# Optimization experiments

Measured on AMD Instinct MI355X. Metric: run time of the kernel, lower is better.

Reference implementation:

```python
import jax, jax.numpy as jnp
import numpy as np

N_HEAD = 16

def setup_inputs() -> dict:
    key = jax.random.key(0)
    k1, k2, k3 = jax.random.split(key, 3)
    B, T, C = 2, 2048, 2048
    x = jax.random.normal(k1, (B, T, C), dtype=jnp.float32)
    # torch Linear weights are [out, in]; init with small scale for stability
    w_attn = jax.random.normal(k2, (3 * C, C), dtype=jnp.float32) * 0.02
    b_attn = jnp.zeros((3 * C,), dtype=jnp.float32)
    w_proj = jax.random.normal(k3, (C, C), dtype=jnp.float32) * 0.02
    b_proj = jnp.zeros((C,), dtype=jnp.float32)
    return {"x": x, "w_attn": w_attn, "b_attn": b_attn, "w_proj": w_proj, "b_proj": b_proj}

def reference(x, w_attn, b_attn, w_proj, b_proj):
    B, T, C = x.shape
    nh = N_HEAD
    hs = C // nh
    # fused QKV projection (torch Linear: x @ W^T + b)
    qkv = x @ w_attn.T + b_attn                      # [B, T, 3C]
    q, k, v = jnp.split(qkv, 3, axis=2)
    # [B, nh, T, hs]
    q = q.reshape(B, T, nh, hs).transpose(0, 2, 1, 3)
    k = k.reshape(B, T, nh, hs).transpose(0, 2, 1, 3)
    v = v.reshape(B, T, nh, hs).transpose(0, 2, 1, 3)
    # causal scaled dot-product attention
    scale = 1.0 / jnp.sqrt(jnp.asarray(hs, dtype=x.dtype))
    logits = jnp.einsum("bhqd,bhkd->bhqk", q, k) * scale  # [B, nh, T, T]
    causal = jnp.tril(jnp.ones((T, T), dtype=bool))
    logits = jnp.where(causal, logits, jnp.finfo(logits.dtype).min)
    attn = jax.nn.softmax(logits, axis=-1)
    y = jnp.einsum("bhqk,bhkd->bhqd", attn, v)       # [B, nh, T, hs]
    y = y.transpose(0, 2, 1, 3).reshape(B, T, C)
    # output projection (resid_dropout is identity in eval / p=0)
    y = y @ w_proj.T + b_proj
    return y
```

## Files before the change

### kernel.cpp

```cpp
#include <hip/hip_runtime.h>
#include <stdint.h>

typedef __bf16 bf16_t;
typedef __bf16 bf16x8 __attribute__((ext_vector_type(8)));
typedef float f32x4 __attribute__((ext_vector_type(4)));
typedef unsigned short us16x8 __attribute__((ext_vector_type(8)));

#define MFMA16(a, b, c) __builtin_amdgcn_mfma_f32_16x16x32_bf16(a, b, c, 0, 0, 0)
#define BAR() __builtin_amdgcn_s_barrier()
#define PRIO1() __builtin_amdgcn_s_setprio(1)
#define PRIO0() __builtin_amdgcn_s_setprio(0)
#define LGKM0()                                        \
  do {                                                 \
    asm volatile("s_waitcnt lgkmcnt(0)" ::: "memory"); \
    __builtin_amdgcn_sched_barrier(0);                 \
  } while (0)
#define VMCNT(n)                                          \
  do {                                                    \
    asm volatile("s_waitcnt vmcnt(" #n ")" ::: "memory"); \
    __builtin_amdgcn_sched_barrier(0);                    \
  } while (0)

__device__ __forceinline__ void stage16(const bf16_t* g, bf16_t* l) {
  __builtin_amdgcn_global_load_lds((__attribute__((address_space(1))) void*)g,
                                   (__attribute__((address_space(3))) void*)l, 16, 0, 0);
}

__global__ __launch_bounds__(256) void cvt_all(const float* __restrict__ x,
                                               const float* __restrict__ wa,
                                               const float* __restrict__ wp,
                                               bf16_t* __restrict__ xb,
                                               bf16_t* __restrict__ wab,
                                               bf16_t* __restrict__ wpb) {
  int i = blockIdx.x * 256 + threadIdx.x;
  const float* src;
  bf16_t* dst;
  if (i < 1048576) {
    src = x + (size_t)i * 8;
    dst = xb + (size_t)i * 8;
  } else if (i < 2621440) {
    size_t j = (size_t)(i - 1048576) * 8;
    src = wa + j;
    dst = wab + j;
  } else {
    size_t j = (size_t)(i - 2621440) * 8;
    src = wp + j;
    dst = wpb + j;
  }
  const f32x4* p = (const f32x4*)src;
  f32x4 a = p[0], b = p[1];
  bf16x8 o;
  o[0] = (bf16_t)a[0]; o[1] = (bf16_t)a[1]; o[2] = (bf16_t)a[2]; o[3] = (bf16_t)a[3];
  o[4] = (bf16_t)b[0]; o[5] = (bf16_t)b[1]; o[6] = (bf16_t)b[2]; o[7] = (bf16_t)b[3];
  *(bf16x8*)dst = o;
}

template <int OUT_BF16>
__global__ __launch_bounds__(256, 2) void gemm_w128p(const bf16_t* __restrict__ A,
                                                     const bf16_t* __restrict__ B,
                                                     const float* __restrict__ bias,
                                                     void* __restrict__ Cout,
                                                     int M, int N, int K) {
  __shared__ bf16_t SA[3 * 256 * 32];
  __shared__ bf16_t SB[3 * 128 * 32];
  const int tid = threadIdx.x;
  const int l = tid & 63, w = tid >> 6;
  const int l15 = l & 15, l4 = l >> 4;
  const int wm = w >> 1, wn = w & 1;
  const int nbn = N >> 7;
  const int nbm = M >> 8;
  const int total = nbm * nbn;
  const int bnpc = nbn >> 3;

  const int r0 = tid >> 2;
  const int scol = (((tid & 3) ^ ((r0 >> 1) & 3)) << 3);
  const size_t K64 = (size_t)64 * K;

  const int swz = (l4 ^ ((l15 >> 1) & 3)) << 3;
  int aoff[8], boff[4];
#pragma unroll
  for (int i = 0; i < 8; ++i) aoff[i] = (wm * 128 + i * 16 + l15) * 32 + swz;
#pragma unroll
  for (int i = 0; i < 4; ++i) boff[i] = (wn * 64 + i * 16 + l15) * 32 + swz;

  const int nk = K >> 5;

  for (int wk = blockIdx.x; wk < total; wk += gridDim.x) {
    const int c = wk & 7, rr0 = wk >> 3;
    const int bm = rr0 / bnpc;
    const int bn = c * bnpc + rr0 % bnpc;

    const bf16_t* gA = A + (size_t)(bm * 256 + r0) * K + scol;
    const bf16_t* gB = B + (size_t)(bn * 128 + r0) * K + scol;

    f32x4 acc[8][4] = {};

    auto STAGE = [&](int t2, int buf) {
      const size_t ko = (size_t)t2 * 32;
      stage16(gA + ko, SA + buf * 8192 + tid * 8);
      stage16(gA + K64 + ko, SA + buf * 8192 + 2048 + tid * 8);
      stage16(gA + 2 * K64 + ko, SA + buf * 8192 + 4096 + tid * 8);
      stage16(gA + 3 * K64 + ko, SA + buf * 8192 + 6144 + tid * 8);
      stage16(gB + ko, SB + buf * 4096 + tid * 8);
      stage16(gB + K64 + ko, SB + buf * 4096 + 2048 + tid * 8);
    };

    auto TILE = [&](int t, int bufR, int bufS) {
      const int t2 = (t + 2 < nk) ? t + 2 : nk - 1;
      STAGE(t2, bufS);
      bf16x8 aR[8], bR[4];
#pragma unroll
      for (int i = 0; i < 8; ++i) aR[i] = *(const bf16x8*)(SA + bufR * 8192 + aoff[i]);
#pragma unroll
      for (int i = 0; i < 4; ++i) bR[i] = *(const bf16x8*)(SB + bufR * 4096 + boff[i]);
      VMCNT(6);
      BAR();
      LGKM0();
      PRIO1();
#pragma unroll
      for (int mi = 0; mi < 8; ++mi)
#pragma unroll
        for (int ni = 0; ni < 4; ++ni)
          acc[mi][ni] = MFMA16(aR[mi], bR[ni], acc[mi][ni]);
      PRIO0();
      BAR();
    };

    STAGE(0, 0);
    STAGE(1, 1);
    VMCNT(6);
    BAR();

    for (int t = 0; t < nk - 1; t += 3) {
      TILE(t, 0, 2);
      TILE(t + 1, 1, 0);
      TILE(t + 2, 2, 1);
    }
    TILE(nk - 1, 0, 2);
    VMCNT(0);

    const int rbase = bm * 256 + wm * 128 + (l4 << 2);
    const int cbase = bn * 128 + wn * 64 + l15;
#pragma unroll
    for (int ni = 0; ni < 4; ++ni) {
      float bv = bias[cbase + ni * 16];
#pragma unroll
      for (int mi = 0; mi < 8; ++mi)
#pragma unroll
        for (int rr = 0; rr < 4; ++rr) {
          float v = acc[mi][ni][rr] + bv;
          size_t off = (size_t)(rbase + mi * 16 + rr) * N + (cbase + ni * 16);
          if (OUT_BF16) ((bf16_t*)Cout)[off] = (bf16_t)v;
          else ((float*)Cout)[off] = v;
        }
    }
  }
}

__global__ __launch_bounds__(256, 2) void attn_fwd(const bf16_t* __restrict__ qkv,
                                                   bf16_t* __restrict__ att) {
  __shared__ bf16_t Kt[2][64 * 128];
  __shared__ bf16_t Vt[2][128 * 64];
  __shared__ bf16_t Pw[4][16 * 64];

  int bid = blockIdx.x;
  int pair = bid >> 5, bh = bid & 31;
  int h = bh & 15, b = bh >> 4;
  int tid = threadIdx.x;
  int l = tid & 63, w = tid >> 6;
  int l15 = l & 15, l4 = l >> 4, l7 = l & 7;
  const size_t LD = 6144;
  const bf16_t* base = qkv + (size_t)b * 2048 * LD;

  us16x8 va[2], vb[2];

  auto loadV = [&](int kb) {
    const bf16_t* vg = base + (size_t)kb * LD + 4096 + h * 128;
#pragma unroll
    for (int p = 0; p < 2; ++p) {
      int g = p * 256 + tid;
      int kvp = (g >> 4) << 1;
      int d0 = (g & 15) << 3;
      va[p] = *(const us16x8*)(vg + (size_t)kvp * LD + d0);
      vb[p] = *(const us16x8*)(vg + (size_t)(kvp + 1) * LD + d0);
    }
  };
  auto stageK = [&](int kb, int buf) {
    const bf16_t* kg = base + (size_t)kb * LD + 2048 + h * 128;
#pragma unroll
    for (int i = 0; i < 4; ++i) {
      int e = i * 256 + tid;
      int row = e >> 4, blk = e & 15;
      int src = (blk ^ (row & 7)) << 3;
      stage16(kg + (size_t)row * LD + src, &Kt[buf][e * 8]);
    }
  };
  auto writeV = [&](int buf) {
#pragma unroll
    for (int p = 0; p < 2; ++p) {
      int g = p * 256 + tid;
      int kvp = (g >> 4) << 1;
      int d0 = (g & 15) << 3;
      int k8 = kvp >> 3, kr = kvp & 7;
#pragma unroll
      for (int j = 0; j < 8; ++j) {
        int d = d0 + j;
        int swzv = k8 ^ ((d ^ (d >> 3)) & 7);
        unsigned pack = (unsigned)va[p][j] | ((unsigned)vb[p][j] << 16);
        *(unsigned*)(&Vt[buf][d * 64 + swzv * 8 + kr]) = pack;
      }
    }
  };

#pragma unroll 1
  for (int phase = 0; phase < 2; ++phase) {
    int qt = phase ? 31 - pair : pair;
    int q0 = qt << 6;
    int wq0 = q0 + w * 16;

    bf16x8 qf[4];
#pragma unroll
    for (int kk = 0; kk < 4; ++kk)
      qf[kk] = *(const bf16x8*)(base + (size_t)(wq0 + l15) * LD + h * 128 + kk * 32 + l4 * 8);

    f32x4 acc[8] = {};
    float mrow[4], lrow[4];
#pragma unroll
    for (int r = 0; r < 4; ++r) { mrow[r] = -1e30f; lrow[r] = 0.f; }

    int nkt = qt + 1;

    loadV(0);
    stageK(0, 0);
    VMCNT(4);
    writeV(0);
    LGKM0();
    VMCNT(0);
    BAR();

#pragma unroll 1
    for (int kt = 0; kt < nkt; ++kt) {
      const int cur = kt & 1, nxt = cur ^ 1;
      const bool pf = (kt + 1 < nkt);
      const int kb = kt << 6;
      if (pf) {
        loadV((kt + 1) << 6);
        stageK((kt + 1) << 6, nxt);
      }

      f32x4 s[4] = {};
      PRIO1();
#pragma unroll
      for (int kk = 0; kk < 4; ++kk) {
        int blk = (kk * 4 + l4) ^ l7;
#pragma unroll
        for (int n = 0; n < 4; ++n) {
          bf16x8 kf = *(const bf16x8*)(&Kt[cur][(n * 16 + l15) * 128 + blk * 8]);
          s[n] = MFMA16(qf[kk], kf, s[n]);
        }
      }
      PRIO0();

      const float sc = 0.08838834764831845f;
      bool needMask = (kb + 63) > wq0;
      float scf[4];
#pragma unroll
      for (int r = 0; r < 4; ++r) {
        int q = wq0 + (l4 << 2) + r;
#pragma unroll
        for (int n = 0; n < 4; ++n) {
          float v = s[n][r] * sc;
          if (needMask && (kb + n * 16 + l15) > q) v = -1e30f;
          s[n][r] = v;
        }
        float mx = fmaxf(fmaxf(s[0][r], s[1][r]), fmaxf(s[2][r], s[3][r]));
        mx = fmaxf(mx, __shfl_xor(mx, 1));
        mx = fmaxf(mx, __shfl_xor(mx, 2));
        mx = fmaxf(mx, __shfl_xor(mx, 4));
        mx = fmaxf(mx, __shfl_xor(mx, 8));
        float mn = fmaxf(mrow[r], mx);
        float sf = __expf(mrow[r] - mn);
        mrow[r] = mn;
        scf[r] = sf;
        float rs = 0.f;
#pragma unroll
        for (int n = 0; n < 4; ++n) {
          float pv = __expf(s[n][r] - mn);
          s[n][r] = pv;
          rs += pv;
        }
        rs += __shfl_xor(rs, 1);
        rs += __shfl_xor(rs, 2);
        rs += __shfl_xor(rs, 4);
        rs += __shfl_xor(rs, 8);
        lrow[r] = lrow[r] * sf + rs;
      }

      if (pf) {
        VMCNT(4);
        writeV(nxt);
      }

#pragma unroll
      for (int nd = 0; nd < 8; ++nd)
#pragma unroll
        for (int r = 0; r < 4; ++r)
          acc[nd][r] *= scf[r];
#pragma unroll
      for (int n = 0; n < 4; ++n) {
        int cb8 = n * 2 + (l15 >> 3);
#pragma unroll
        for (int r = 0; r < 4; ++r) {
          int row = (l4 << 2) + r;
          Pw[w][row * 64 + ((cb8 ^ (row & 7)) << 3) + l7] = (bf16_t)s[n][r];
        }
      }

      PRIO1();
#pragma unroll
      for (int kk2 = 0; kk2 < 2; ++kk2) {
        bf16x8 pa = *(const bf16x8*)(&Pw[w][l15 * 64 + (((kk2 * 4 + l4) ^ l7) << 3)]);
#pragma unroll
        for (int nd = 0; nd < 8; ++nd) {
          int d = nd * 16 + l15;
          int swzv = (kk2 * 4 + l4) ^ ((d ^ (d >> 3)) & 7);
          bf16x8 bv = *(const bf16x8*)(&Vt[cur][d * 64 + swzv * 8]);
          acc[nd] = MFMA16(pa, bv, acc[nd]);
        }
      }
      PRIO0();

      LGKM0();
      VMCNT(0);
      BAR();
    }

#pragma unroll
    for (int r = 0; r < 4; ++r) {
      float inv = 1.0f / lrow[r];
      size_t ro = (size_t)(b * 2048 + wq0 + (l4 << 2) + r) * 2048 + h * 128;
#pragma unroll
      for (int nd = 0; nd < 8; ++nd)
        att[ro + nd * 16 + l15] = (bf16_t)(acc[nd][r] * inv);
    }
  }
}

extern "C" void kernel_launch(void* const* d_in, const int* in_sizes, int n_in,
                              void* d_out, int out_size, void* d_ws, size_t ws_size,
                              hipStream_t stream) {
  (void)in_sizes; (void)n_in; (void)out_size; (void)ws_size;
  const float* x = (const float*)d_in[0];
  const float* w_attn = (const float*)d_in[1];
  const float* b_attn = (const float*)d_in[2];
  const float* w_proj = (const float*)d_in[3];
  const float* b_proj = (const float*)d_in[4];
  float* out = (float*)d_out;

  char* ws = (char*)d_ws;
  bf16_t* xb  = (bf16_t*)(ws);
  bf16_t* wab = (bf16_t*)(ws + 16777216);
  bf16_t* wpb = (bf16_t*)(ws + 41943040);
  bf16_t* qkv = (bf16_t*)(ws + 50331648);
  bf16_t* att = xb;

  cvt_all<<<12288, 256, 0, stream>>>(x, w_attn, w_proj, xb, wab, wpb);

  gemm_w128p<1><<<512, 256, 0, stream>>>(xb, wab, b_attn, qkv, 4096, 6144, 2048);

  attn_fwd<<<512, 256, 0, stream>>>(qkv, att);

  gemm_w128p<0><<<256, 256, 0, stream>>>(att, wpb, b_proj, out, 4096, 2048, 2048);
}
```

Baseline: 296.9 us.

## Use 128-row query tiles per block and drop double-buffered K/V pipeline

The attention kernel now gives each block one 128-row query tile, with each wave holding 32 rows (two 16-row MFMA tiles), so every K/V fragment read from LDS is reused across two query tiles. The old two-phase pairing of 64-row tiles and the double-buffered asynchronous K/V prefetch are replaced by a single-buffered load, sync, compute loop, and the P scratch uses padded rows instead of an XOR swizzle. Blocks are balanced by pairing query tile p with 15-p across the grid halves. The output-projection GEMM launch grid is doubled. The cost is that K/V load latency is no longer overlapped with compute, and waves whose rows lie entirely above the causal diagonal sit idle on the last tile.

```diff
diff --git a/kernel.cpp b/kernel.cpp
--- a/kernel.cpp
+++ b/kernel.cpp
@@ -159,191 +159,169 @@
 
 __global__ __launch_bounds__(256, 2) void attn_fwd(const bf16_t* __restrict__ qkv,
                                                    bf16_t* __restrict__ att) {
-  __shared__ bf16_t Kt[2][64 * 128];
-  __shared__ bf16_t Vt[2][128 * 64];
-  __shared__ bf16_t Pw[4][16 * 64];
+  __shared__ bf16_t Kt[64 * 128];
+  __shared__ bf16_t Vt[128 * 64];
+  __shared__ bf16_t Pl[4][32 * 72];
 
   int bid = blockIdx.x;
-  int pair = bid >> 5, bh = bid & 31;
+  int bh = bid & 31;
   int h = bh & 15, b = bh >> 4;
+  int p = (bid >> 5) & 7;
+  int qt = (bid >> 8) ? 15 - p : p;
   int tid = threadIdx.x;
   int l = tid & 63, w = tid >> 6;
   int l15 = l & 15, l4 = l >> 4, l7 = l & 7;
+  int q0 = qt << 7, wq0 = q0 + w * 32;
   const size_t LD = 6144;
   const bf16_t* base = qkv + (size_t)b * 2048 * LD;
 
-  us16x8 va[2], vb[2];
-
-  auto loadV = [&](int kb) {
+  bf16x8 qf[2][4];
+#pragma unroll
+  for (int m2 = 0; m2 < 2; ++m2)
+#pragma unroll
+    for (int kk = 0; kk < 4; ++kk)
+      qf[m2][kk] = *(const bf16x8*)(base + (size_t)(wq0 + m2 * 16 + l15) * LD +
+                                    h * 128 + kk * 32 + l4 * 8);
+
+  f32x4 acc[2][8] = {};
+  float mrow[2][4], lrow[2][4];
+#pragma unroll
+  for (int m2 = 0; m2 < 2; ++m2)
+#pragma unroll
+    for (int r = 0; r < 4; ++r) { mrow[m2][r] = -1e30f; lrow[m2][r] = 0.f; }
+
+  int nkt = 2 * qt + 2;
+#pragma unroll 1
+  for (int kt = 0; kt < nkt; ++kt) {
+    int kb = kt << 6;
     const bf16_t* vg = base + (size_t)kb * LD + 4096 + h * 128;
-#pragma unroll
-    for (int p = 0; p < 2; ++p) {
-      int g = p * 256 + tid;
-      int kvp = (g >> 4) << 1;
+    us16x8 va[2], vb[2];
+#pragma unroll
+    for (int pp = 0; pp < 2; ++pp) {
+      int g = pp * 256 + tid;
+      int kv = (g >> 4) << 1;
       int d0 = (g & 15) << 3;
-      va[p] = *(const us16x8*)(vg + (size_t)kvp * LD + d0);
-      vb[p] = *(const us16x8*)(vg + (size_t)(kvp + 1) * LD + d0);
-    }
-  };
-  auto stageK = [&](int kb, int buf) {
+      va[pp] = *(const us16x8*)(vg + (size_t)kv * LD + d0);
+      vb[pp] = *(const us16x8*)(vg + (size_t)(kv + 1) * LD + d0);
+    }
     const bf16_t* kg = base + (size_t)kb * LD + 2048 + h * 128;
 #pragma unroll
     for (int i = 0; i < 4; ++i) {
       int e = i * 256 + tid;
       int row = e >> 4, blk = e & 15;
       int src = (blk ^ (row & 7)) << 3;
-      stage16(kg + (size_t)row * LD + src, &Kt[buf][e * 8]);
-    }
-  };
-  auto writeV = [&](int buf) {
-#pragma unroll
-    for (int p = 0; p < 2; ++p) {
-      int g = p * 256 + tid;
-      int kvp = (g >> 4) << 1;
+      stage16(kg + (size_t)row * LD + src, Kt + e * 8);
+    }
+#pragma unroll
+    for (int pp = 0; pp < 2; ++pp) {
+      int g = pp * 256 + tid;
+      int kv = (g >> 4) << 1;
       int d0 = (g & 15) << 3;
-      int k8 = kvp >> 3, kr = kvp & 7;
+      int k8 = kv >> 3, kr = kv & 7;
 #pragma unroll
       for (int j = 0; j < 8; ++j) {
         int d = d0 + j;
         int swzv = k8 ^ ((d ^ (d >> 3)) & 7);
-        unsigned pack = (unsigned)va[p][j] | ((unsigned)vb[p][j] << 16);
-        *(unsigned*)(&Vt[buf][d * 64 + swzv * 8 + kr]) = pack;
+        unsigned pack = (unsigned)va[pp][j] | ((unsigned)vb[pp][j] << 16);
+        *(unsigned*)(&Vt[d * 64 + swzv * 8 + kr]) = pack;
       }
     }
-  };
-
-#pragma unroll 1
-  for (int phase = 0; phase < 2; ++phase) {
-    int qt = phase ? 31 - pair : pair;
-    int q0 = qt << 6;
-    int wq0 = q0 + w * 16;
-
-    bf16x8 qf[4];
-#pragma unroll
-    for (int kk = 0; kk < 4; ++kk)
-      qf[kk] = *(const bf16x8*)(base + (size_t)(wq0 + l15) * LD + h * 128 + kk * 32 + l4 * 8);
-
-    f32x4 acc[8] = {};
-    float mrow[4], lrow[4];
-#pragma unroll
-    for (int r = 0; r < 4; ++r) { mrow[r] = -1e30f; lrow[r] = 0.f; }
-
-    int nkt = qt + 1;
-
-    loadV(0);
-    stageK(0, 0);
-    VMCNT(4);
-    writeV(0);
-    LGKM0();
-    VMCNT(0);
-    BAR();
-
-#pragma unroll 1
-    for (int kt = 0; kt < nkt; ++kt) {
-      const int cur = kt & 1, nxt = cur ^ 1;
-      const bool pf = (kt + 1 < nkt);
-      const int kb = kt << 6;
-      if (pf) {
-        loadV((kt + 1) << 6);
-        stageK((kt + 1) << 6, nxt);
-      }
-
-      f32x4 s[4] = {};
+    __syncthreads();
+
+    if (kb < wq0 + 32) {
+      bool needMask = (kb + 63) > wq0;
+      f32x4 s[2][4] = {};
       PRIO1();
 #pragma unroll
       for (int kk = 0; kk < 4; ++kk) {
         int blk = (kk * 4 + l4) ^ l7;
 #pragma unroll
         for (int n = 0; n < 4; ++n) {
-          bf16x8 kf = *(const bf16x8*)(&Kt[cur][(n * 16 + l15) * 128 + blk * 8]);
-          s[n] = MFMA16(qf[kk], kf, s[n]);
+          bf16x8 kf = *(const bf16x8*)(Kt + (n * 16 + l15) * 128 + blk * 8);
+          s[0][n] = MFMA16(qf[0][kk], kf, s[0][n]);
+          s[1][n] = MFMA16(qf[1][kk], kf, s[1][n]);
         }
       }
       PRIO0();
-
       const float sc = 0.08838834764831845f;
-      bool needMask = (kb + 63) > wq0;
-      float scf[4];
-#pragma unroll
-      for (int r = 0; r < 4; ++r) {
-        int q = wq0 + (l4 << 2) + r;
-#pragma unroll
-        for (int n = 0; n < 4; ++n) {
-          float v = s[n][r] * sc;
-          if (needMask && (kb + n * 16 + l15) > q) v = -1e30f;
-          s[n][r] = v;
-        }
-        float mx = fmaxf(fmaxf(s[0][r], s[1][r]), fmaxf(s[2][r], s[3][r]));
-        mx = fmaxf(mx, __shfl_xor(mx, 1));
-        mx = fmaxf(mx, __shfl_xor(mx, 2));
-        mx = fmaxf(mx, __shfl_xor(mx, 4));
-        mx = fmaxf(mx, __shfl_xor(mx, 8));
-        float mn = fmaxf(mrow[r], mx);
-        float sf = __expf(mrow[r] - mn);
-        mrow[r] = mn;
-        scf[r] = sf;
-        float rs = 0.f;
-#pragma unroll
-        for (int n = 0; n < 4; ++n) {
-          float pv = __expf(s[n][r] - mn);
-          s[n][r] = pv;
-          rs += pv;
-        }
-        rs += __shfl_xor(rs, 1);
-        rs += __shfl_xor(rs, 2);
-        rs += __shfl_xor(rs, 4);
-        rs += __shfl_xor(rs, 8);
-        lrow[r] = lrow[r] * sf + rs;
-      }
-
-      if (pf) {
-        VMCNT(4);
-        writeV(nxt);
-      }
-
-#pragma unroll
-      for (int nd = 0; nd < 8; ++nd)
-#pragma unroll
-        for (int r = 0; r < 4; ++r)
-          acc[nd][r] *= scf[r];
-#pragma unroll
-      for (int n = 0; n < 4; ++n) {
-        int cb8 = n * 2 + (l15 >> 3);
+      float scf[2][4];
+#pragma unroll
+      for (int m2 = 0; m2 < 2; ++m2) {
 #pragma unroll
         for (int r = 0; r < 4; ++r) {
-          int row = (l4 << 2) + r;
-          Pw[w][row * 64 + ((cb8 ^ (row & 7)) << 3) + l7] = (bf16_t)s[n][r];
+          int q = wq0 + m2 * 16 + (l4 << 2) + r;
+#pragma unroll
+          for (int n = 0; n < 4; ++n) {
+            float v = s[m2][n][r] * sc;
+            if (needMask && (kb + n * 16 + l15) > q) v = -1e30f;
+            s[m2][n][r] = v;
+          }
+          float mx = fmaxf(fmaxf(s[m2][0][r], s[m2][1][r]), fmaxf(s[m2][2][r], s[m2][3][r]));
+          mx = fmaxf(mx, __shfl_xor(mx, 1));
+          mx = fmaxf(mx, __shfl_xor(mx, 2));
+          mx = fmaxf(mx, __shfl_xor(mx, 4));
+          mx = fmaxf(mx, __shfl_xor(mx, 8));
+          float mn = fmaxf(mrow[m2][r], mx);
+          float sf = __expf(mrow[m2][r] - mn);
+          mrow[m2][r] = mn;
+          scf[m2][r] = sf;
+          float rs = 0.f;
+#pragma unroll
+          for (int n = 0; n < 4; ++n) {
+            float pv = __expf(s[m2][n][r] - mn);
+            s[m2][n][r] = pv;
+            rs += pv;
+          }
+          rs += __shfl_xor(rs, 1);
+          rs += __shfl_xor(rs, 2);
+          rs += __shfl_xor(rs, 4);
+          rs += __shfl_xor(rs, 8);
+          lrow[m2][r] = lrow[m2][r] * sf + rs;
         }
       }
-
+#pragma unroll
+      for (int m2 = 0; m2 < 2; ++m2)
+#pragma unroll
+        for (int nd = 0; nd < 8; ++nd)
+#pragma unroll
+          for (int r = 0; r < 4; ++r)
+            acc[m2][nd][r] *= scf[m2][r];
+#pragma unroll
+      for (int m2 = 0; m2 < 2; ++m2)
+#pragma unroll
+        for (int n = 0; n < 4; ++n)
+#pragma unroll
+          for (int r = 0; r < 4; ++r)
+            Pl[w][(m2 * 16 + (l4 << 2) + r) * 72 + n * 16 + l15] = (bf16_t)s[m2][n][r];
       PRIO1();
 #pragma unroll
       for (int kk2 = 0; kk2 < 2; ++kk2) {
-        bf16x8 pa = *(const bf16x8*)(&Pw[w][l15 * 64 + (((kk2 * 4 + l4) ^ l7) << 3)]);
+        bf16x8 pa0 = *(const bf16x8*)(&Pl[w][l15 * 72 + kk2 * 32 + l4 * 8]);
+        bf16x8 pa1 = *(const bf16x8*)(&Pl[w][(16 + l15) * 72 + kk2 * 32 + l4 * 8]);
 #pragma unroll
         for (int nd = 0; nd < 8; ++nd) {
           int d = nd * 16 + l15;
           int swzv = (kk2 * 4 + l4) ^ ((d ^ (d >> 3)) & 7);
-          bf16x8 bv = *(const bf16x8*)(&Vt[cur][d * 64 + swzv * 8]);
-          acc[nd] = MFMA16(pa, bv, acc[nd]);
+          bf16x8 bv = *(const bf16x8*)(&Vt[d * 64 + swzv * 8]);
+          acc[0][nd] = MFMA16(pa0, bv, acc[0][nd]);
+          acc[1][nd] = MFMA16(pa1, bv, acc[1][nd]);
         }
       }
       PRIO0();
-
-      LGKM0();
-      VMCNT(0);
-      BAR();
-    }
-
+    }
+    __syncthreads();
+  }
+
+#pragma unroll
+  for (int m2 = 0; m2 < 2; ++m2)
 #pragma unroll
     for (int r = 0; r < 4; ++r) {
-      float inv = 1.0f / lrow[r];
-      size_t ro = (size_t)(b * 2048 + wq0 + (l4 << 2) + r) * 2048 + h * 128;
+      float inv = 1.0f / lrow[m2][r];
+      size_t ro = (size_t)(b * 2048 + wq0 + m2 * 16 + (l4 << 2) + r) * 2048 + h * 128;
 #pragma unroll
       for (int nd = 0; nd < 8; ++nd)
-        att[ro + nd * 16 + l15] = (bf16_t)(acc[nd][r] * inv);
-    }
-  }
+        att[ro + nd * 16 + l15] = (bf16_t)(acc[m2][nd][r] * inv);
+    }
 }
 
 extern "C" void kernel_launch(void* const* d_in, const int* in_sizes, int n_in,
@@ -370,5 +348,5 @@
 
   attn_fwd<<<512, 256, 0, stream>>>(qkv, att);
 
-  gemm_w128p<0><<<256, 256, 0, stream>>>(att, wpb, b_proj, out, 4096, 2048, 2048);
-}
+  gemm_w128p<0><<<512, 256, 0, stream>>>(att, wpb, b_proj, out, 4096, 2048, 2048);
+}
```

Result: slower. 316.5 us (+6.6%).
